# Performance work log

Hardware: AMD Instinct MI355X
Metric: run time of the kernel (lower is better)

Reference implementation:

```python
import jax, jax.numpy as jnp
import numpy as np

P = 8          # patch_size
EPS = 1e-6     # LayerNorm2d eps


def _conv(x, w, b, groups=1):
    # x: (B,Cin,H,W), w: (Cout, Cin//groups, kh, kw)
    y = jax.lax.conv_general_dilated(
        x, w, window_strides=(1, 1), padding='SAME',
        feature_group_count=groups,
        dimension_numbers=('NCHW', 'OIHW', 'NCHW'))
    return y + b[None, :, None, None]


def _ln2d(x, w, b):
    mu = jnp.mean(x, axis=1, keepdims=True)
    var = jnp.mean((x - mu) ** 2, axis=1, keepdims=True)
    y = (x - mu) / jnp.sqrt(var + EPS)
    return w[None, :, None, None] * y + b[None, :, None, None]


def _fft_mix(x, fw):
    # windowed rFFT2 -> per-(channel,freq) real weight -> irFFT2.
    # H,W divisible by P, so window_partitionx == plain window partition.
    B, C, H, W = x.shape
    nh, nw = H // P, W // P
    xw = x.reshape(B, C, nh, P, nw, P).transpose(0, 2, 4, 1, 3, 5)  # (B,nh,nw,C,P,P)
    f = jnp.fft.rfft2(xw)                    # (B,nh,nw,C,P,P//2+1)
    f = f * fw                               # fw: (C,P,P//2+1) broadcasts
    xw = jnp.fft.irfft2(f, s=(P, P))
    return xw.transpose(0, 3, 1, 4, 2, 5).reshape(B, C, H, W)


def _gelu(x):
    return jax.nn.gelu(x, approximate=False)  # torch nn.GELU default = exact erf


def setup_inputs() -> dict:
    key = jax.random.key(0)
    ks = jax.random.split(key, 18)
    B, C, H, W = 4, 64, 256, 256
    C4, D = C * 4, C // 4
    f32 = jnp.float32

    def n(k, shape, s):
        return (jax.random.normal(k, shape, f32) * s)

    return {
        'x': jax.random.normal(ks[0], (B, C, H, W), f32),
        'ln_w': jnp.ones((C,), f32),
        'ln_b': jnp.zeros((C,), f32),
        'pconv_w': n(ks[1], (D, D, 3, 3), 0.08),
        'pconv_b': n(ks[2], (D,), 0.02),
        'w0': n(ks[3], (C4, C, 1, 1), 0.12),
        'b0': n(ks[4], (C4,), 0.02),
        'w1': n(ks[5], (C4, C, 1, 1), 0.12),
        'b1': n(ks[6], (C4,), 0.02),
        'w2': n(ks[7], (C, C4, 1, 1), 0.06),
        'b2': n(ks[8], (C,), 0.02),
        'w3': n(ks[9], (C4, 1, 3, 3), 0.3),
        'b3': n(ks[10], (C4,), 0.02),
        'w4': n(ks[11], (C, C4, 1, 1), 0.06),
        'b4': n(ks[12], (C,), 0.02),
        'fftw1': 1.0 + n(ks[13], (C, P, P // 2 + 1), 0.1),
        'fftw2': 1.0 + n(ks[14], (C, P, P // 2 + 1), 0.1),
    }


def reference(x, ln_w, ln_b, pconv_w, pconv_b, w0, b0, w1, b1,
              w2, b2, w3, b3, w4, b4, fftw1, fftw2):
    C = x.shape[1]
    D = C // 4
    C4 = C * 4

    xn = _ln2d(x, ln_w, ln_b)

    # partial 3x3 conv on first C//4 channels
    y1 = _conv(xn[:, :D], pconv_w, pconv_b)
    x2 = jnp.concatenate([y1, xn[:, D:]], axis=1)

    # branch 1: 1x1 expand -> GELU -> 1x1 contract -> windowed FFT mixing
    x1 = _conv(xn, w0, b0)
    x1 = _gelu(x1)
    x1 = _conv(x1, w2, b2)
    x1 = _fft_mix(x1, fftw1)

    # branch 2: 1x1 expand -> GELU -> depthwise 3x3 -> GELU -> 1x1 contract -> FFT mixing
    x2 = _conv(x2, w1, b1)
    x2 = _gelu(x2)
    x2 = _conv(x2, w3, b3, groups=C4)
    x2 = _gelu(x2)
    x2 = _conv(x2, w4, b4)
    x2 = _fft_mix(x2, fftw2)

    return x1 + x2
```

## Files before the change

kernel.cpp:

```cpp
#include <hip/hip_runtime.h>


typedef _Float16 f16;
typedef _Float16 f16x2 __attribute__((ext_vector_type(2)));
typedef _Float16 f16x4 __attribute__((ext_vector_type(4)));
typedef _Float16 f16x8 __attribute__((ext_vector_type(8)));
typedef float f32x4 __attribute__((ext_vector_type(4)));

__device__ __forceinline__ float gelu_f(float x) {
  float u = 1.5957691216f * (x + 0.044715f * x * x * x);
  float t = exp2f(-1.4426950409f * u);
#if __has_builtin(__builtin_amdgcn_rcpf)
  return x * __builtin_amdgcn_rcpf(1.0f + t);
#else
  return x / (1.0f + t);
#endif
}

__device__ __forceinline__ float dot2f(f16x2 a, f16x2 b, float c) {
#if __has_builtin(__builtin_amdgcn_fdot2)
  return __builtin_amdgcn_fdot2(a, b, c, false);
#else
  return c + (float)a.x * (float)b.x + (float)a.y * (float)b.y;
#endif
}

__global__ void build_kappa_kernel(const float* __restrict__ fw1,
                                   const float* __restrict__ fw2,
                                   float* __restrict__ kap1,
                                   float* __restrict__ kap2) {
  int which = blockIdx.x >> 6, c = blockIdx.x & 63;
  const float* fw = which ? fw2 : fw1;
  float* kap = which ? kap2 : kap1;
  int t = threadIdx.x, a = t >> 3, bb = t & 7;
  __shared__ float Wt[64];
  __shared__ float ct[8];
  if (t == 0) {
    const float r2 = 0.70710678118654752440f;
    ct[0] = 1.f; ct[1] = r2; ct[2] = 0.f; ct[3] = -r2;
    ct[4] = -1.f; ct[5] = -r2; ct[6] = 0.f; ct[7] = r2;
  }
  {
    int u = a, v = bb;
    Wt[t] = (v <= 4) ? fw[c * 40 + u * 5 + v]
                     : fw[c * 40 + ((8 - u) & 7) * 5 + (8 - v)];
  }
  __syncthreads();
  float acc = 0.f;
  for (int u = 0; u < 8; ++u)
    for (int v = 0; v < 8; ++v)
      acc += Wt[u * 8 + v] * ct[(u * a + v * bb) & 7];
  kap[c * 64 + t] = acc * 0.015625f;
}

__global__ void preconv_kernel(const float* __restrict__ w0, const float* __restrict__ w1,
                               const float* __restrict__ w2, const float* __restrict__ w4,
                               const float* __restrict__ w3, const float* __restrict__ b3,
                               f16* __restrict__ W0h, f16* __restrict__ W1h,
                               f16* __restrict__ W2h, f16* __restrict__ W4h,
                               f16* __restrict__ w3pk, f16* __restrict__ b3pk) {
  int i = blockIdx.x * 256 + threadIdx.x;
  if (i < 16384) W0h[i] = (f16)w0[i];
  else if (i < 32768) W1h[i - 16384] = (f16)w1[i - 16384];
  else if (i < 49152) W2h[i - 32768] = (f16)w2[i - 32768];
  else if (i < 65536) W4h[i - 49152] = (f16)w4[i - 49152];
  else if (i < 67840) {
    int j = i - 65536;
    int g = j / 72, r = j % 72, tap = r >> 3, k = r & 7;
    w3pk[j] = (f16)w3[(g * 8 + k) * 9 + tap];
  } else if (i < 68096) {
    int k = i - 67840;
    b3pk[k] = (f16)b3[k];
  }
}

__global__ void __launch_bounds__(256) ln_kernel(const float* __restrict__ x,
                                                 const float* __restrict__ lnw,
                                                 const float* __restrict__ lnb,
                                                 f16* __restrict__ xn) {
  int b = blockIdx.y;
  int px = blockIdx.x * 256 + threadIdx.x;
  const float* xp = x + ((size_t)b << 22) + px;
  float v[64];
  float s = 0.f;
#pragma unroll
  for (int c = 0; c < 64; ++c) { v[c] = xp[(size_t)c << 16]; s += v[c]; }
  float mu = s * (1.f / 64.f), s2 = 0.f;
#pragma unroll
  for (int c = 0; c < 64; ++c) { float d = v[c] - mu; s2 += d * d; }
  float rstd = rsqrtf(s2 * (1.f / 64.f) + 1e-6f);
  f16* op = xn + (size_t)b * 4194304 + (size_t)px * 64;
#pragma unroll
  for (int g = 0; g < 8; ++g) {
    f16x8 pk;
#pragma unroll
    for (int j = 0; j < 8; ++j) {
      int c = g * 8 + j;
      pk[j] = (f16)((v[c] - mu) * rstd * lnw[c] + lnb[c]);
    }
    *(f16x8*)(op + g * 8) = pk;
  }
}

__global__ void __launch_bounds__(256) pconv_kernel(const f16* __restrict__ xn,
                                                    const float* __restrict__ pw,
                                                    const float* __restrict__ pb,
                                                    f16* __restrict__ y1) {
  __shared__ __align__(16) char halo[18 * 640];
  __shared__ f16 wpk[2304];
  __shared__ float pbs[16];
  int t = threadIdx.x, blk = blockIdx.x, b = blockIdx.y;
  const f16* xnb = xn + (size_t)b * 4194304;
  f16* y1b = y1 + (size_t)b * 1048576;
  int h0 = (blk >> 4) << 4, w0 = (blk & 15) << 4;
  for (int i = t; i < 2304; i += 256) {
    int co = i / 144, r = i % 144, tap = r >> 4, ci = r & 15;
    wpk[i] = (f16)pw[co * 144 + ci * 9 + tap];
  }
  if (t < 16) pbs[t] = pb[t];
  for (int i = 0; i < 3; ++i) {
    int u = i * 256 + t;
    if (u < 648) {
      int hp = u >> 1, half = u & 1;
      int hr = hp / 18, hc = hp - hr * 18;
      int h = h0 - 1 + hr, w = w0 - 1 + hc;
      f16x8 v = {0, 0, 0, 0, 0, 0, 0, 0};
      if ((unsigned)h < 256u && (unsigned)w < 256u)
        v = *(const f16x8*)(xnb + ((((size_t)h << 8)) + w) * 64 + half * 8);
      *(f16x8*)(halo + hr * 640 + ((hc * 32 + half * 16) ^ ((hr & 7) << 4))) = v;
    }
  }
  __syncthreads();
  int rl = t >> 4, cl = t & 15;
  float acc[16];
#pragma unroll
  for (int co = 0; co < 16; ++co) acc[co] = pbs[co];
#pragma unroll
  for (int ty = 0; ty < 3; ++ty)
#pragma unroll
    for (int tx = 0; tx < 3; ++tx) {
      int hr = rl + ty, hc = cl + tx, tap = ty * 3 + tx;
      f16x8 ld0 = *(const f16x8*)(halo + hr * 640 + ((hc * 32) ^ ((hr & 7) << 4)));
      f16x8 ld1 = *(const f16x8*)(halo + hr * 640 + ((hc * 32 + 16) ^ ((hr & 7) << 4)));
#pragma unroll
      for (int co = 0; co < 16; ++co) {
#pragma unroll
        for (int p = 0; p < 4; ++p) {
          f16x2 xp = {ld0[2 * p], ld0[2 * p + 1]};
          f16x2 wp = *(const f16x2*)&wpk[co * 144 + tap * 16 + 2 * p];
          acc[co] = dot2f(xp, wp, acc[co]);
        }
#pragma unroll
        for (int p = 0; p < 4; ++p) {
          f16x2 xp = {ld1[2 * p], ld1[2 * p + 1]};
          f16x2 wp = *(const f16x2*)&wpk[co * 144 + tap * 16 + 8 + 2 * p];
          acc[co] = dot2f(xp, wp, acc[co]);
        }
      }
    }
  size_t px = (((size_t)(h0 + rl)) << 8) + w0 + cl;
  f16x8 o0, o1;
#pragma unroll
  for (int j = 0; j < 8; ++j) { o0[j] = (f16)acc[j]; o1[j] = (f16)acc[8 + j]; }
  *(f16x8*)(y1b + px * 16) = o0;
  *(f16x8*)(y1b + px * 16 + 8) = o1;
}

__global__ void __launch_bounds__(256) b1_kernel(
    const f16* __restrict__ xn, const f16* __restrict__ W0h,
    const float* __restrict__ b0, const f16* __restrict__ W2h,
    const float* __restrict__ b2, f16* __restrict__ u1d,
    f16* __restrict__ u1w) {
  __shared__ __align__(16) f16 As[8192];
  __shared__ __align__(16) f16 Es[8192];
  int t = threadIdx.x, b = blockIdx.y;
  const f16* xnb = xn + (size_t)b * 4194304;
  f16* u1b = (b < 3) ? (u1d + (size_t)b * 4194304) : u1w;
  int px0 = blockIdx.x << 7;
#pragma unroll
  for (int i = 0; i < 4; ++i) {
    int u = i * 256 + t, row = u >> 3, cb = (u & 7) << 4;
    f16x8 v = *(const f16x8*)(xnb + (size_t)(px0 + row) * 64 + (cb >> 1));
    *(f16x8*)((char*)As + row * 128 + (cb ^ ((row & 7) << 4))) = v;
  }
  __syncthreads();
  int l = t & 63, wv = t >> 6, lm = l & 15, kg = l >> 4;
  f32x4 uacc[2][4];
#pragma unroll
  for (int a = 0; a < 2; ++a)
#pragma unroll
    for (int n = 0; n < 4; ++n) uacc[a][n] = (f32x4){0.f, 0.f, 0.f, 0.f};
  for (int cc = 0; cc < 4; ++cc) {
    f32x4 eacc[2][4];
#pragma unroll
    for (int a = 0; a < 2; ++a)
#pragma unroll
      for (int n = 0; n < 4; ++n) eacc[a][n] = (f32x4){0.f, 0.f, 0.f, 0.f};
#pragma unroll
    for (int kk = 0; kk < 2; ++kk) {
      int kb = kk * 64 + kg * 16;
      f16x8 af[2];
#pragma unroll
      for (int mt = 0; mt < 2; ++mt) {
        int row = wv * 32 + mt * 16 + lm;
        af[mt] = *(const f16x8*)((char*)As + row * 128 + (kb ^ ((row & 7) << 4)));
      }
      f16x8 bf[4];
#pragma unroll
      for (int nt = 0; nt < 4; ++nt) {
        int co = cc * 64 + nt * 16 + lm;
        bf[nt] = *(const f16x8*)(W0h + (size_t)co * 64 + kk * 32 + kg * 8);
      }
#pragma unroll
      for (int mt = 0; mt < 2; ++mt)
#pragma unroll
        for (int nt = 0; nt < 4; ++nt)
          eacc[mt][nt] = __builtin_amdgcn_mfma_f32_16x16x32_f16(bf[nt], af[mt], eacc[mt][nt], 0, 0, 0);
    }
    if (cc) __syncthreads();
#pragma unroll
    for (int mt = 0; mt < 2; ++mt) {
      int row = wv * 32 + mt * 16 + lm;
#pragma unroll
      for (int nt = 0; nt < 4; ++nt) {
        int c0 = nt * 16 + kg * 4;
        float4 bz4 = *(const float4*)&b0[cc * 64 + c0];
        f16x4 pk;
        pk[0] = (f16)gelu_f(eacc[mt][nt][0] + bz4.x);
        pk[1] = (f16)gelu_f(eacc[mt][nt][1] + bz4.y);
        pk[2] = (f16)gelu_f(eacc[mt][nt][2] + bz4.z);
        pk[3] = (f16)gelu_f(eacc[mt][nt][3] + bz4.w);
        *(f16x4*)((char*)Es + row * 128 + ((c0 * 2) ^ ((row & 7) << 4))) = pk;
      }
    }
    __syncthreads();
#pragma unroll
    for (int kk = 0; kk < 2; ++kk) {
      int kb = kk * 64 + kg * 16;
      f16x8 af[2];
#pragma unroll
      for (int mt = 0; mt < 2; ++mt) {
        int row = wv * 32 + mt * 16 + lm;
        af[mt] = *(const f16x8*)((char*)Es + row * 128 + (kb ^ ((row & 7) << 4)));
      }
      f16x8 bf[4];
#pragma unroll
      for (int nt = 0; nt < 4; ++nt) {
        int co = nt * 16 + lm;
        bf[nt] = *(const f16x8*)(W2h + (size_t)co * 256 + cc * 64 + kk * 32 + kg * 8);
      }
#pragma unroll
      for (int mt = 0; mt < 2; ++mt)
#pragma unroll
        for (int nt = 0; nt < 4; ++nt)
          uacc[mt][nt] = __builtin_amdgcn_mfma_f32_16x16x32_f16(bf[nt], af[mt], uacc[mt][nt], 0, 0, 0);
    }
    __syncthreads();
  }
#pragma unroll
  for (int mt = 0; mt < 2; ++mt) {
    int row = wv * 32 + mt * 16 + lm;
#pragma unroll
    for (int nt = 0; nt < 4; ++nt) {
      int c0 = nt * 16 + kg * 4;
      float4 bz4 = *(const float4*)&b2[c0];
      f16x4 pk;
      pk[0] = (f16)(uacc[mt][nt][0] + bz4.x);
      pk[1] = (f16)(uacc[mt][nt][1] + bz4.y);
      pk[2] = (f16)(uacc[mt][nt][2] + bz4.z);
      pk[3] = (f16)(uacc[mt][nt][3] + bz4.w);
      *(f16x4*)((char*)Es + row * 128 + ((c0 * 2) ^ ((row & 7) << 4))) = pk;
    }
  }
  __syncthreads();
  int co = t >> 2, q = t & 3;
  f16x8 o[4];
#pragma unroll
  for (int i = 0; i < 32; ++i) {
    int m = q * 32 + i;
    o[i >> 3][i & 7] =
        *(const f16*)((char*)Es + m * 128 + ((co * 2) ^ ((m & 7) << 4)));
  }
  f16* up = u1b + ((size_t)co << 16) + px0 + q * 32;
#pragma unroll
  for (int ss = 0; ss < 4; ++ss) *(f16x8*)(up + ss * 8) = o[ss];
}

__global__ void __launch_bounds__(256) b2_kernel(
    const f16* __restrict__ xn, const f16* __restrict__ y1,
    const f16* __restrict__ W1h, const float* __restrict__ b1v,
    const f16* __restrict__ W4h, const float* __restrict__ b4,
    const f16* __restrict__ w3pk, const f16* __restrict__ b3pk,
    f16* __restrict__ u2) {
  __shared__ __align__(16) f16 xin[12288];
  __shared__ __align__(16) f16 Es[6144];
  __shared__ __align__(16) f16 Gs[4096];
  __shared__ __align__(16) f16 w3s[2304];
  __shared__ __align__(16) f16 b3s[256];
  int t = threadIdx.x, blk = blockIdx.x, b = blockIdx.y;
  const f16* xnb = xn + (size_t)b * 4194304;
  const f16* y1b = y1 + (size_t)b * 1048576;
  f16* u2b = u2 + (size_t)b * 4194304;
  int h0 = (blk >> 4) << 3, w0 = (blk & 15) << 4;
  for (int i = t; i < 288; i += 256)
    *(f16x8*)(w3s + i * 8) = *(const f16x8*)(w3pk + i * 8);
  if (t < 32) *(f16x8*)(b3s + t * 8) = *(const f16x8*)(b3pk + t * 8);
#pragma unroll
  for (int i = 0; i < 6; ++i) {
    int u = i * 256 + t;
    int hp = u >> 3, part = u & 7;
    f16x8 v = {0, 0, 0, 0, 0, 0, 0, 0};
    if (hp < 180) {
      int hr = hp / 18, hc = hp - hr * 18;
      int h = h0 - 1 + hr, w = w0 - 1 + hc;
      if ((unsigned)h < 256u && (unsigned)w < 256u) {
        size_t px = ((size_t)h << 8) + w;
        v = (part < 2) ? *(const f16x8*)(y1b + px * 16 + part * 8)
                       : *(const f16x8*)(xnb + px * 64 + part * 8);
      }
    }
    *(f16x8*)((char*)xin + hp * 128 + ((part * 16) ^ ((hp & 7) << 4))) = v;
  }
  __syncthreads();
  int l = t & 63, wv = t >> 6, lm = l & 15, kg = l >> 4;
  int pxl = t & 127, chh = t >> 7, rl = pxl >> 4, cl = pxl & 15;
  f32x4 uacc[2][4];
#pragma unroll
  for (int a = 0; a < 2; ++a)
#pragma unroll
    for (int n = 0; n < 4; ++n) uacc[a][n] = (f32x4){0.f, 0.f, 0.f, 0.f};
  for (int kc = 0; kc < 4; ++kc) {
#pragma unroll
    for (int sub = 0; sub < 2; ++sub) {
      int ce0 = kc * 64 + sub * 32;
      f32x4 eacc[3][2];
#pragma unroll
      for (int a = 0; a < 3; ++a)
#pragma unroll
        for (int n = 0; n < 2; ++n) eacc[a][n] = (f32x4){0.f, 0.f, 0.f, 0.f};
#pragma unroll
      for (int kk = 0; kk < 2; ++kk) {
        int kb = kk * 64 + kg * 16;
        f16x8 af[3];
#pragma unroll
        for (int mtl = 0; mtl < 3; ++mtl) {
          int row = (mtl * 4 + wv) * 16 + lm;
          af[mtl] = *(const f16x8*)((char*)xin + row * 128 + (kb ^ ((row & 7) << 4)));
        }
        f16x8 bf[2];
#pragma unroll
        for (int nt = 0; nt < 2; ++nt) {
          int ce = ce0 + nt * 16 + lm;
          bf[nt] = *(const f16x8*)(W1h + (size_t)ce * 64 + kk * 32 + kg * 8);
        }
#pragma unroll
        for (int mtl = 0; mtl < 3; ++mtl)
#pragma unroll
          for (int nt = 0; nt < 2; ++nt)
            eacc[mtl][nt] = __builtin_amdgcn_mfma_f32_16x16x32_f16(bf[nt], af[mtl], eacc[mtl][nt], 0, 0, 0);
      }
#pragma unroll
      for (int mtl = 0; mtl < 3; ++mtl) {
        int row = (mtl * 4 + wv) * 16 + lm;
#pragma unroll
        for (int nt = 0; nt < 2; ++nt) {
          int cL = nt * 16 + kg * 4;
          float4 bz4 = *(const float4*)&b1v[ce0 + cL];
          f16x4 pk;
          pk[0] = (f16)gelu_f(eacc[mtl][nt][0] + bz4.x);
          pk[1] = (f16)gelu_f(eacc[mtl][nt][1] + bz4.y);
          pk[2] = (f16)gelu_f(eacc[mtl][nt][2] + bz4.z);
          pk[3] = (f16)gelu_f(eacc[mtl][nt][3] + bz4.w);
          *(f16x4*)((char*)Es + row * 64 + ((cL * 2) ^ (((row >> 1) & 3) << 4))) = pk;
        }
      }
      __syncthreads();
#pragma unroll
      for (int c8 = 0; c8 < 2; ++c8) {
        int ceL = chh * 16 + c8 * 8;
        int ceG = ce0 + ceL, g9 = ceG >> 3;
        f16x8 a8 = *(const f16x8*)(b3s + ceG);
#pragma unroll
        for (int ty = 0; ty < 3; ++ty)
#pragma unroll
          for (int tx = 0; tx < 3; ++tx) {
            int hp = (rl + ty) * 18 + (cl + tx);
            f16x8 xv = *(const f16x8*)((char*)Es + hp * 64 + ((ceL * 2) ^ (((hp >> 1) & 3) << 4)));
            f16x8 wv8 = *(const f16x8*)(w3s + g9 * 72 + (ty * 3 + tx) * 8);
            a8 += xv * wv8;
          }
        f16x8 r8;
#pragma unroll
        for (int j2 = 0; j2 < 8; ++j2) r8[j2] = (f16)gelu_f((float)a8[j2]);
        *(f16x8*)((char*)Gs + pxl * 64 + ((ceL * 2) ^ (((pxl >> 1) & 3) << 4))) = r8;
      }
      __syncthreads();
      f16x8 af2[2];
#pragma unroll
      for (int mt = 0; mt < 2; ++mt) {
        int row = wv * 32 + mt * 16 + lm;
        af2[mt] = *(const f16x8*)((char*)Gs + row * 64 + ((kg * 16) ^ (((row >> 1) & 3) << 4)));
      }
      f16x8 bf2[4];
#pragma unroll
      for (int nt = 0; nt < 4; ++nt) {
        int co = nt * 16 + lm;
        bf2[nt] = *(const f16x8*)(W4h + (size_t)co * 256 + ce0 + kg * 8);
      }
#pragma unroll
      for (int mt = 0; mt < 2; ++mt)
#pragma unroll
        for (int nt = 0; nt < 4; ++nt)
          uacc[mt][nt] = __builtin_amdgcn_mfma_f32_16x16x32_f16(bf2[nt], af2[mt], uacc[mt][nt], 0, 0, 0);
      __syncthreads();
    }
  }
#pragma unroll
  for (int mt = 0; mt < 2; ++mt) {
    int m = wv * 32 + mt * 16 + lm;
#pragma unroll
    for (int nt = 0; nt < 4; ++nt) {
      int c0 = nt * 16 + kg * 4;
      float4 bz4 = *(const float4*)&b4[c0];
      f16x4 pk;
      pk[0] = (f16)(uacc[mt][nt][0] + bz4.x);
      pk[1] = (f16)(uacc[mt][nt][1] + bz4.y);
      pk[2] = (f16)(uacc[mt][nt][2] + bz4.z);
      pk[3] = (f16)(uacc[mt][nt][3] + bz4.w);
      *(f16x4*)((char*)xin + m * 128 + ((c0 * 2) ^ ((m & 7) << 4))) = pk;
    }
  }
  __syncthreads();
  int co = t >> 2, q = t & 3;
  f16x8 o[4];
#pragma unroll
  for (int i = 0; i < 32; ++i) {
    int m = q * 32 + i;
    o[i >> 3][i & 7] =
        *(const f16*)((char*)xin + m * 128 + ((co * 2) ^ ((m & 7) << 4)));
  }
  f16* up = u2b + ((size_t)co << 16) + (size_t)(h0 + 2 * q) * 256 + w0;
  *(f16x8*)(up) = o[0];
  *(f16x8*)(up + 8) = o[1];
  *(f16x8*)(up + 256) = o[2];
  *(f16x8*)(up + 256 + 8) = o[3];
}

__global__ void __launch_bounds__(256) fftmix_kernel(
    const f16* __restrict__ u1, const f16* __restrict__ u2,
    const float* __restrict__ kap1, const float* __restrict__ kap2,
    float* __restrict__ out, int b) {
  int blk = blockIdx.x;
  int c = blk >> 3, part = blk & 7;
  int t = threadIdx.x;
  int l = t & 63, wv = (t >> 6) & 3;
  int s = l >> 3, tq = l & 7;
  __shared__ unsigned int kls[64];
  if (t < 64) {
    f16 k1 = (f16)kap1[(c << 6) + t];
    f16 k2 = (f16)kap2[(c << 6) + t];
    kls[t] = (unsigned int)__builtin_bit_cast(unsigned short, k1) |
             ((unsigned int)__builtin_bit_cast(unsigned short, k2) << 16);
  }
  __syncthreads();
  unsigned int kp[64];
#pragma unroll
  for (int j = 0; j < 64; ++j) {
    int idx = (((s - (j >> 3)) & 7) << 3) | ((tq - (j & 7)) & 7);
    kp[j] = kls[idx];
  }
  size_t cb = ((size_t)c) << 16;
  size_t obase = ((size_t)(b * 64 + c)) << 16;
  int win0 = part * 128 + wv * 32;
  for (int it = 0; it < 32; ++it) {
    int win = win0 + it;
    int wh = win >> 5, ww = win & 31;
    size_t pix = (size_t)((wh * 8 + s) << 8) + ww * 8 + tq;
    unsigned int pk =
        (unsigned int)__builtin_bit_cast(unsigned short, u1[cb + pix]) |
        ((unsigned int)__builtin_bit_cast(unsigned short, u2[cb + pix]) << 16);
    float acc = 0.f;
#pragma unroll
    for (int j = 0; j < 64; ++j) {
      unsigned int bc = (unsigned int)__builtin_amdgcn_readlane((int)pk, j);
      acc = dot2f(__builtin_bit_cast(f16x2, bc),
                  __builtin_bit_cast(f16x2, kp[j]), acc);
    }
    out[obase + pix] = acc;
  }
}

__global__ void diag_kernel(float* __restrict__ out, float code, int n) {
  int i = blockIdx.x * 256 + threadIdx.x;
  for (int p = i; p < n; p += 256 * 4096) out[p] = (p == 0) ? code : 0.f;
}

extern "C" void kernel_launch(void* const* d_in, const int* in_sizes, int n_in,
                              void* d_out, int out_size, void* d_ws,
                              size_t ws_size, hipStream_t stream) {
  const float* x       = (const float*)d_in[0];
  const float* ln_w    = (const float*)d_in[1];
  const float* ln_b    = (const float*)d_in[2];
  const float* pconv_w = (const float*)d_in[3];
  const float* pconv_b = (const float*)d_in[4];
  const float* w0      = (const float*)d_in[5];
  const float* b0      = (const float*)d_in[6];
  const float* w1      = (const float*)d_in[7];
  const float* b1      = (const float*)d_in[8];
  const float* w2      = (const float*)d_in[9];
  const float* b2      = (const float*)d_in[10];
  const float* w3      = (const float*)d_in[11];
  const float* b3      = (const float*)d_in[12];
  const float* w4      = (const float*)d_in[13];
  const float* b4      = (const float*)d_in[14];
  const float* fftw1   = (const float*)d_in[15];
  const float* fftw2   = (const float*)d_in[16];

  const size_t OFF_KAP1 = 0;
  const size_t OFF_KAP2 = 16384;
  const size_t OFF_W0H  = 32768;
  const size_t OFF_W1H  = 65536;
  const size_t OFF_W2H  = 98304;
  const size_t OFF_W4H  = 131072;
  const size_t OFF_W3PK = 163840;
  const size_t OFF_B3PK = 168448;
  const size_t OFF_Y1   = 168960;
  const size_t OFF_U2   = OFF_Y1 + 8388608ull;
  const size_t OFF_U13  = OFF_U2 + 33554432ull;
  const size_t WS_NEED  = OFF_U13 + 8388608ull;

  float* outF = (float*)d_out;
  if (ws_size < WS_NEED) {
    diag_kernel<<<4096, 256, 0, stream>>>(outF, 1000.0f + (float)(ws_size >> 20), 16777216);
    return;
  }
  char* ws = (char*)d_ws;
  float* kap1 = (float*)(ws + OFF_KAP1);
  float* kap2 = (float*)(ws + OFF_KAP2);
  f16* W0h  = (f16*)(ws + OFF_W0H);
  f16* W1h  = (f16*)(ws + OFF_W1H);
  f16* W2h  = (f16*)(ws + OFF_W2H);
  f16* W4h  = (f16*)(ws + OFF_W4H);
  f16* w3pk = (f16*)(ws + OFF_W3PK);
  f16* b3pk = (f16*)(ws + OFF_B3PK);
  f16* Y1   = (f16*)(ws + OFF_Y1);
  f16* U2   = (f16*)(ws + OFF_U2);
  f16* U13  = (f16*)(ws + OFF_U13);

  f16* XN  = (f16*)d_out;
  f16* U1D = (f16*)d_out + 16777216;

  build_kappa_kernel<<<128, 64, 0, stream>>>(fftw1, fftw2, kap1, kap2);
  preconv_kernel<<<266, 256, 0, stream>>>(w0, w1, w2, w4, w3, b3,
                                          W0h, W1h, W2h, W4h, w3pk, b3pk);
  ln_kernel<<<dim3(256, 4), 256, 0, stream>>>(x, ln_w, ln_b, XN);
  pconv_kernel<<<dim3(256, 4), 256, 0, stream>>>(XN, pconv_w, pconv_b, Y1);
  b1_kernel<<<dim3(512, 4), 256, 0, stream>>>(XN, W0h, b0, W2h, b2, U1D, U13);
  b2_kernel<<<dim3(512, 4), 256, 0, stream>>>(XN, Y1, W1h, b1, W4h, b4,
                                              w3pk, b3pk, U2);
  for (int b = 0; b < 4; ++b) {
    const f16* u1b = (b < 3) ? (U1D + (size_t)b * 4194304) : U13;
    fftmix_kernel<<<512, 256, 0, stream>>>(u1b, U2 + (size_t)b * 4194304,
                                           kap1, kap2, outF, b);
  }
}
```

Measured before the change: 405.2 us.

## Compute depthwise conv directly into MFMA operand registers, drop Gs staging

Each thread now computes the depthwise 3x3 conv plus GELU for exactly the pixels and channels it needs as the A-operand of the contract MFMA, writing the result straight into registers instead of through the Gs shared buffer. The Gs buffer, the w3/b3 shared copies and one barrier per sub-iteration go away, and depthwise weights are read from global/L1 per sub-step. Shared memory footprint shrinks, which may allow more resident blocks. The thread-to-work mapping of the depthwise stage changes, which may change LDS access patterns and the number of registers in use.

```diff
diff --git a/kernel.cpp b/kernel.cpp
--- a/kernel.cpp
+++ b/kernel.cpp
@@ -294,17 +294,11 @@
     f16* __restrict__ u2) {
   __shared__ __align__(16) f16 xin[12288];
   __shared__ __align__(16) f16 Es[6144];
-  __shared__ __align__(16) f16 Gs[4096];
-  __shared__ __align__(16) f16 w3s[2304];
-  __shared__ __align__(16) f16 b3s[256];
   int t = threadIdx.x, blk = blockIdx.x, b = blockIdx.y;
   const f16* xnb = xn + (size_t)b * 4194304;
   const f16* y1b = y1 + (size_t)b * 1048576;
   f16* u2b = u2 + (size_t)b * 4194304;
   int h0 = (blk >> 4) << 3, w0 = (blk & 15) << 4;
-  for (int i = t; i < 288; i += 256)
-    *(f16x8*)(w3s + i * 8) = *(const f16x8*)(w3pk + i * 8);
-  if (t < 32) *(f16x8*)(b3s + t * 8) = *(const f16x8*)(b3pk + t * 8);
 #pragma unroll
   for (int i = 0; i < 6; ++i) {
     int u = i * 256 + t;
@@ -323,7 +317,6 @@
   }
   __syncthreads();
   int l = t & 63, wv = t >> 6, lm = l & 15, kg = l >> 4;
-  int pxl = t & 127, chh = t >> 7, rl = pxl >> 4, cl = pxl & 15;
   f32x4 uacc[2][4];
 #pragma unroll
   for (int a = 0; a < 2; ++a)
@@ -359,6 +352,7 @@
           for (int nt = 0; nt < 2; ++nt)
             eacc[mtl][nt] = __builtin_amdgcn_mfma_f32_16x16x32_f16(bf[nt], af[mtl], eacc[mtl][nt], 0, 0, 0);
       }
+      __syncthreads();
 #pragma unroll
       for (int mtl = 0; mtl < 3; ++mtl) {
         int row = (mtl * 4 + wv) * 16 + lm;
@@ -375,31 +369,28 @@
         }
       }
       __syncthreads();
-#pragma unroll
-      for (int c8 = 0; c8 < 2; ++c8) {
-        int ceL = chh * 16 + c8 * 8;
-        int ceG = ce0 + ceL, g9 = ceG >> 3;
-        f16x8 a8 = *(const f16x8*)(b3s + ceG);
+      int g9 = (ce0 + kg * 8) >> 3;
+      f16x8 wv9[9];
+#pragma unroll
+      for (int tap = 0; tap < 9; ++tap)
+        wv9[tap] = *(const f16x8*)(w3pk + g9 * 72 + tap * 8);
+      f16x8 bias8 = *(const f16x8*)(b3pk + ce0 + kg * 8);
+      f16x8 af2[2];
+#pragma unroll
+      for (int mt = 0; mt < 2; ++mt) {
+        int px = wv * 32 + mt * 16 + lm;
+        int rl2 = px >> 4, cl2 = px & 15;
+        f16x8 a8 = bias8;
 #pragma unroll
         for (int ty = 0; ty < 3; ++ty)
 #pragma unroll
           for (int tx = 0; tx < 3; ++tx) {
-            int hp = (rl + ty) * 18 + (cl + tx);
-            f16x8 xv = *(const f16x8*)((char*)Es + hp * 64 + ((ceL * 2) ^ (((hp >> 1) & 3) << 4)));
-            f16x8 wv8 = *(const f16x8*)(w3s + g9 * 72 + (ty * 3 + tx) * 8);
-            a8 += xv * wv8;
+            int hp = (rl2 + ty) * 18 + (cl2 + tx);
+            f16x8 xv = *(const f16x8*)((char*)Es + hp * 64 + ((kg * 16) ^ (((hp >> 1) & 3) << 4)));
+            a8 += xv * wv9[ty * 3 + tx];
           }
-        f16x8 r8;
-#pragma unroll
-        for (int j2 = 0; j2 < 8; ++j2) r8[j2] = (f16)gelu_f((float)a8[j2]);
-        *(f16x8*)((char*)Gs + pxl * 64 + ((ceL * 2) ^ (((pxl >> 1) & 3) << 4))) = r8;
-      }
-      __syncthreads();
-      f16x8 af2[2];
-#pragma unroll
-      for (int mt = 0; mt < 2; ++mt) {
-        int row = wv * 32 + mt * 16 + lm;
-        af2[mt] = *(const f16x8*)((char*)Gs + row * 64 + ((kg * 16) ^ (((row >> 1) & 3) << 4)));
+#pragma unroll
+        for (int j2 = 0; j2 < 8; ++j2) af2[mt][j2] = (f16)gelu_f((float)a8[j2]);
       }
       f16x8 bf2[4];
 #pragma unroll
@@ -412,9 +403,9 @@
 #pragma unroll
         for (int nt = 0; nt < 4; ++nt)
           uacc[mt][nt] = __builtin_amdgcn_mfma_f32_16x16x32_f16(bf2[nt], af2[mt], uacc[mt][nt], 0, 0, 0);
-      __syncthreads();
-    }
-  }
+    }
+  }
+  __syncthreads();
 #pragma unroll
   for (int mt = 0; mt < 2; ++mt) {
     int m = wv * 32 + mt * 16 + lm;
```

Measured after the change: 395.3 us. 1.03x faster.
